# Kernel optimization log

Measured on AMD Instinct MI355X. Metric: run time of the kernel, lower is better.

Reference implementation:

```python
import jax, jax.numpy as jnp
import numpy as np

NEG = -1e30


def setup_inputs() -> dict:
    key = jax.random.key(0)
    k1, k2, k3, k4 = jax.random.split(key, 4)
    B, L, T, M = 64, 256, 1600, 80
    probs = jax.random.uniform(k1, (B, L, T), dtype=jnp.float32)
    melspec = jax.random.normal(k2, (B, M, T), dtype=jnp.float32)
    text_lengths = jax.random.randint(k3, (B,), 1, L + 1)   # values in [1, L]
    mel_lengths = jax.random.randint(k4, (B,), 1, T + 1)    # values in [1, T]
    return {"probs": probs, "melspec": melspec,
            "text_lengths": text_lengths, "mel_lengths": mel_lengths}


def reference(probs, melspec, text_lengths, mel_lengths):
    B, L, _ = probs.shape
    T = melspec.shape[2]
    log_prob_matrix = jnp.log(probs + 1e-30)            # [B, L, T]
    lp_t = jnp.moveaxis(log_prob_matrix, 2, 0)          # [T, B, L]

    # t = 0: only (l=0, t=0) is alive
    init = jnp.full((B, L), NEG, dtype=log_prob_matrix.dtype)
    init = init.at[:, 0].set(lp_t[0, :, 0])

    def step(prev, lp):
        # stay at label l, or advance from label l-1 (monotonic alignment)
        shifted = jnp.concatenate(
            [jnp.full((B, 1), NEG, dtype=prev.dtype), prev[:, :-1]], axis=1)
        new = jnp.logaddexp(prev, shifted) + lp
        return new, new

    _, ys = jax.lax.scan(step, init, lp_t[1:])          # ys: [T-1, B, L]
    log_alpha = jnp.concatenate([init[None], ys], axis=0)  # [T, B, L]

    b = jnp.arange(B)
    alpha_last = log_alpha[mel_lengths - 1, b, text_lengths - 1]  # [B]
    mdn_loss = -alpha_last.mean()
    return (mdn_loss, log_prob_matrix)
```

## Files before the change

### kernel.cpp

```cpp
#include <hip/hip_runtime.h>

#define LN2f 0.69314718055994531f

constexpr int T_C  = 1600;
constexpr int L_C  = 256;
constexpr int DP_B = 64;
constexpr int CK   = 16;
constexpr int LOGB = 1216;

typedef float f4u __attribute__((ext_vector_type(4), aligned(4)));
typedef float f4a __attribute__((ext_vector_type(4)));

__device__ __forceinline__ float shift_up1_f(float x, bool f15, bool f31) {
    int xi  = __float_as_int(x);
    int s   = __builtin_amdgcn_update_dpp(0, xi, 0x111, 0xF, 0xF, true);
    int b15 = __builtin_amdgcn_update_dpp(0, xi, 0x142, 0xF, 0xF, true);
    int b31 = __builtin_amdgcn_update_dpp(0, xi, 0x143, 0xF, 0xF, true);
    int r = f15 ? b15 : s;
    r     = f31 ? b31 : r;
    return __int_as_float(r);
}
__device__ __forceinline__ int shift_up1_i(int x, bool f15, bool f31) {
    int s   = __builtin_amdgcn_update_dpp(0, x, 0x111, 0xF, 0xF, true);
    int b15 = __builtin_amdgcn_update_dpp(0, x, 0x142, 0xF, 0xF, true);
    int b31 = __builtin_amdgcn_update_dpp(0, x, 0x143, 0xF, 0xF, true);
    int r = f15 ? b15 : s;
    r     = f31 ? b31 : r;
    return r;
}

__global__ __launch_bounds__(256, 5) void fused_kernel(
    const float* __restrict__ probs,
    const int* __restrict__ text_len,
    const int* __restrict__ mel_len,
    float* __restrict__ out1,
    float* __restrict__ alpha_out,
    int n4)
{
    __shared__ float lds[2][CK][L_C];
    const int b   = blockIdx.x;
    const int tid = threadIdx.x;

    if (b >= DP_B) {
        const int W = LOGB * 256;
        const int M = n4 - 1;
        int m = (b - DP_B) * 256 + tid;
        if (m >= M) return;
        const float* src = probs + 3;
        float*       dst = out1 + 3;
        f4u v0 = *(const f4u*)(src + 4 * (size_t)m);
        int  m1 = m + W;
        bool h1 = m1 < M;
        f4u v1 = v0;
        if (h1) v1 = *(const f4u*)(src + 4 * (size_t)m1);
        for (;;) {
            const int  m2 = m1 + W;
            const bool h2 = m2 < M;
            f4u v2;
            if (h2) v2 = *(const f4u*)(src + 4 * (size_t)m2);
            f4a o;
            o.x = __logf(v0.x + 1e-30f);
            o.y = __logf(v0.y + 1e-30f);
            o.z = __logf(v0.z + 1e-30f);
            o.w = __logf(v0.w + 1e-30f);
            __builtin_nontemporal_store(o, (f4a*)(dst + 4 * (size_t)m));
            if (!h1) return;
            v0 = v1; v1 = v2; m = m1; m1 = m2; h1 = h2;
        }
    }

    const int wv   = tid >> 6;
    const int lane = tid & 63;
    const int ml1  = mel_len[b] - 1;
    const int trip = (ml1 >> 4) + 1;

    if (wv != 0) {
        asm volatile("s_setprio 1");
        const int pw   = wv - 1;
        const int q    = lane & 3;
        const int g    = lane >> 2;
        const int row0 = pw * 16 + g;
        const int NIT  = (pw == 0) ? 6 : 5;
        const float* gbase = probs + (size_t)b * (L_C * T_C)
                           + (size_t)row0 * T_C + q * 4;
        const int swz = 8 * q;

        float4 rA[6], rB[6];
        auto LD = [&](float4 (&r)[6], int ck) {
            const float* p = gbase + ck * CK;
#pragma unroll
            for (int it = 0; it < 6; ++it)
                if (it < NIT) r[it] = *(const float4*)(p + it * (48 * T_C));
        };
        auto WR = [&](float4 (&r)[6], int bb) {
            float* Lw = &lds[bb][0][0];
#pragma unroll
            for (int it = 0; it < 6; ++it) {
                if (it < NIT) {
                    const int A0 = q * 1024 + ((row0 + 48 * it) ^ swz);
                    Lw[A0]             = r[it].x + 1e-30f;
                    Lw[A0 + 256]       = r[it].y + 1e-30f;
                    Lw[(A0 ^ 4) + 512] = r[it].z + 1e-30f;
                    Lw[(A0 ^ 4) + 768] = r[it].w + 1e-30f;
                }
            }
        };

        LD(rA, 0);
        if (trip > 1) LD(rB, 1);
        WR(rA, 0);
        for (int w = 0; w < trip; ++w) {
            __syncthreads();
            if ((w & 1) == 0) {
                if (w + 2 < trip) LD(rA, w + 2);
                if (w + 1 < trip) WR(rB, 1);
            } else {
                if (w + 2 < trip) LD(rB, w + 2);
                if (w + 1 < trip) WR(rA, 0);
            }
        }
        return;
    }

    asm volatile("s_setprio 3");
    const int  cl  = text_len[b] - 1;
    const bool f15 = (lane == 16) | (lane == 48);
    const bool f31 = (lane == 32);
    const int  xr  = 4 * lane;

    float a0 = 0.f, a1 = 0.f, a2 = 0.f, a3 = 0.f;
    int   E = 0;
    bool  alive = (lane == 0);
    float s0 = 0.f, s1 = 0.f, s2 = 0.f, s3 = 0.f;
    int   sE = 0;

    auto renorm = [&]() {
        float m = fmaxf(fmaxf(a0, a1), fmaxf(a2, a3));
        int e = ((__float_as_int(m) >> 23) & 255) - 127;
        e = (m > 0.0f) ? e : 0;
        a0 = ldexpf(a0, -e); a1 = ldexpf(a1, -e);
        a2 = ldexpf(a2, -e); a3 = ldexpf(a3, -e);
        E += e;
    };

    for (int w = 0; w < trip; ++w) {
        __syncthreads();
        const float* Lr = &lds[w & 1][0][0];
        const int tb = w << 4;

        auto ldc = [&](int j) -> float4 {
            return *(const float4*)(Lr + j * 256 + (xr ^ (4 * ((j >> 1) & 7))));
        };
        auto step_full = [&](int j) {
            const float4 c = ldc(j);
            float top = shift_up1_f(a3, f15, f31);
            int   tE  = shift_up1_i(E, f15, f31);
            float contrib = alive ? ldexpf(top, tE - E) : top;
            E = alive ? E : tE;
            alive = alive | (top != 0.0f);
            float n0 = (a0 + contrib) * c.x;
            float n1 = (a1 + a0) * c.y;
            float n2 = (a2 + a1) * c.z;
            float n3 = (a3 + a2) * c.w;
            a0 = n0; a1 = n1; a2 = n2; a3 = n3;
            if (tb + j == ml1) { s0 = a0; s1 = a1; s2 = a2; s3 = a3; sE = E; }
        };

        if (w == 0) {
            const float4 c = ldc(0);
            a0 = (lane == 0) ? c.x : 0.0f;
            if (ml1 == 0) s0 = a0;
#pragma unroll
            for (int j = 1; j < CK; ++j) step_full(j);
            renorm();
        } else if (w < 16) {
#pragma unroll
            for (int j = 0; j < CK; ++j) step_full(j);
            renorm();
        } else {
            const int tE = shift_up1_i(E, f15, f31);
            const int dE = tE - E;
            if (w == trip - 1) {
#pragma unroll
                for (int j = 0; j < CK; ++j) {
                    const float4 c = ldc(j);
                    float top = shift_up1_f(a3, f15, f31);
                    float contrib = ldexpf(top, dE);
                    float n0 = (a0 + contrib) * c.x;
                    float n1 = (a1 + a0) * c.y;
                    float n2 = (a2 + a1) * c.z;
                    float n3 = (a3 + a2) * c.w;
                    a0 = n0; a1 = n1; a2 = n2; a3 = n3;
                    if (tb + j == ml1) { s0 = a0; s1 = a1; s2 = a2; s3 = a3; sE = E; }
                }
            } else {
#pragma unroll
                for (int j = 0; j < CK; ++j) {
                    const float4 c = ldc(j);
                    float top = shift_up1_f(a3, f15, f31);
                    float contrib = ldexpf(top, dE);
                    float n0 = (a0 + contrib) * c.x;
                    float n1 = (a1 + a0) * c.y;
                    float n2 = (a2 + a1) * c.z;
                    float n3 = (a3 + a2) * c.w;
                    a0 = n0; a1 = n1; a2 = n2; a3 = n3;
                }
            }
            renorm();
        }
    }

    if (lane == (cl >> 2)) {
        const int jj = cl & 3;
        float v = (jj == 0) ? s0 : (jj == 1) ? s1 : (jj == 2) ? s2 : s3;
        v = fmaxf(v, 1e-44f);
        const float res = (log2f(v) + (float)sE) * LN2f;
        alpha_out[b] = (cl > ml1) ? -1e30f : res;
    }
}

__global__ void loss_kernel(const float* __restrict__ alpha,
                            const float* __restrict__ probs,
                            float* __restrict__ out, int B, int n) {
    const int t = threadIdx.x;
    if (t < 3)  out[1 + t] = __logf(probs[t] + 1e-30f);
    if (t == 3) out[n] = __logf(probs[n - 1] + 1e-30f);
    float v = (t < B) ? alpha[t] : 0.0f;
#pragma unroll
    for (int off = 32; off > 0; off >>= 1) v += __shfl_down(v, off, 64);
    if (t == 0) out[0] = -v / (float)B;
}

extern "C" void kernel_launch(void* const* d_in, const int* in_sizes, int n_in,
                              void* d_out, int out_size, void* d_ws, size_t ws_size,
                              hipStream_t stream) {
    const float* probs    = (const float*)d_in[0];
    const int*   text_len = (const int*)d_in[2];
    const int*   mel_len  = (const int*)d_in[3];
    float* out = (float*)d_out;

    const int B  = in_sizes[2];
    const int n  = in_sizes[0];
    const int n4 = n / 4;
    const int G  = DP_B + LOGB;

    fused_kernel<<<G, 256, 0, stream>>>(probs, text_len, mel_len,
                                        out + 1, (float*)d_ws, n4);
    loss_kernel<<<1, 64, 0, stream>>>((const float*)d_ws, probs, out, B, n);
}
```

Baseline: 270.2 us.

## Deepen producer prefetch to three register stages and batch LDS reads per chunk

The producer waves now keep three register buffers of global loads in flight, prefetching chunk w+3 instead of w+2, so more global latency is hidden behind the serial DP wave. The consumer wave loads all 16 LDS float4 columns of a chunk into registers up front, behind a scheduling barrier, instead of reading each inside the dependent recurrence step. This takes LDS latency off the serial critical path. In exchange, register pressure rises in both roles, which could cause spills or hurt occupancy under the 256x5 launch bounds.

```diff
diff --git a/kernel.cpp b/kernel.cpp
--- a/kernel.cpp
+++ b/kernel.cpp
@@ -85,7 +85,7 @@
                            + (size_t)row0 * T_C + q * 4;
         const int swz = 8 * q;
 
-        float4 rA[6], rB[6];
+        float4 rA[6], rB[6], rC[6];
         auto LD = [&](float4 (&r)[6], int ck) {
             const float* p = gbase + ck * CK;
 #pragma unroll
@@ -108,16 +108,23 @@
 
         LD(rA, 0);
         if (trip > 1) LD(rB, 1);
+        if (trip > 2) LD(rC, 2);
         WR(rA, 0);
+        int ph = 0;
         for (int w = 0; w < trip; ++w) {
             __syncthreads();
-            if ((w & 1) == 0) {
-                if (w + 2 < trip) LD(rA, w + 2);
-                if (w + 1 < trip) WR(rB, 1);
+            const int bb = (w + 1) & 1;
+            if (ph == 0) {
+                if (w + 3 < trip) LD(rA, w + 3);
+                if (w + 1 < trip) WR(rB, bb);
+            } else if (ph == 1) {
+                if (w + 3 < trip) LD(rB, w + 3);
+                if (w + 1 < trip) WR(rC, bb);
             } else {
-                if (w + 2 < trip) LD(rB, w + 2);
-                if (w + 1 < trip) WR(rA, 0);
+                if (w + 3 < trip) LD(rC, w + 3);
+                if (w + 1 < trip) WR(rA, bb);
             }
+            ph = (ph == 2) ? 0 : ph + 1;
         }
         return;
     }
@@ -148,27 +155,28 @@
         const float* Lr = &lds[w & 1][0][0];
         const int tb = w << 4;
 
-        auto ldc = [&](int j) -> float4 {
-            return *(const float4*)(Lr + j * 256 + (xr ^ (4 * ((j >> 1) & 7))));
-        };
+        float4 c[CK];
+#pragma unroll
+        for (int j = 0; j < CK; ++j)
+            c[j] = *(const float4*)(Lr + j * 256 + (xr ^ (4 * ((j >> 1) & 7))));
+        __builtin_amdgcn_sched_barrier(0);
+
         auto step_full = [&](int j) {
-            const float4 c = ldc(j);
             float top = shift_up1_f(a3, f15, f31);
             int   tE  = shift_up1_i(E, f15, f31);
             float contrib = alive ? ldexpf(top, tE - E) : top;
             E = alive ? E : tE;
             alive = alive | (top != 0.0f);
-            float n0 = (a0 + contrib) * c.x;
-            float n1 = (a1 + a0) * c.y;
-            float n2 = (a2 + a1) * c.z;
-            float n3 = (a3 + a2) * c.w;
+            float n0 = (a0 + contrib) * c[j].x;
+            float n1 = (a1 + a0) * c[j].y;
+            float n2 = (a2 + a1) * c[j].z;
+            float n3 = (a3 + a2) * c[j].w;
             a0 = n0; a1 = n1; a2 = n2; a3 = n3;
             if (tb + j == ml1) { s0 = a0; s1 = a1; s2 = a2; s3 = a3; sE = E; }
         };
 
         if (w == 0) {
-            const float4 c = ldc(0);
-            a0 = (lane == 0) ? c.x : 0.0f;
+            a0 = (lane == 0) ? c[0].x : 0.0f;
             if (ml1 == 0) s0 = a0;
 #pragma unroll
             for (int j = 1; j < CK; ++j) step_full(j);
@@ -183,26 +191,24 @@
             if (w == trip - 1) {
 #pragma unroll
                 for (int j = 0; j < CK; ++j) {
-                    const float4 c = ldc(j);
                     float top = shift_up1_f(a3, f15, f31);
                     float contrib = ldexpf(top, dE);
-                    float n0 = (a0 + contrib) * c.x;
-                    float n1 = (a1 + a0) * c.y;
-                    float n2 = (a2 + a1) * c.z;
-                    float n3 = (a3 + a2) * c.w;
+                    float n0 = (a0 + contrib) * c[j].x;
+                    float n1 = (a1 + a0) * c[j].y;
+                    float n2 = (a2 + a1) * c[j].z;
+                    float n3 = (a3 + a2) * c[j].w;
                     a0 = n0; a1 = n1; a2 = n2; a3 = n3;
                     if (tb + j == ml1) { s0 = a0; s1 = a1; s2 = a2; s3 = a3; sE = E; }
                 }
             } else {
 #pragma unroll
                 for (int j = 0; j < CK; ++j) {
-                    const float4 c = ldc(j);
                     float top = shift_up1_f(a3, f15, f31);
                     float contrib = ldexpf(top, dE);
-                    float n0 = (a0 + contrib) * c.x;
-                    float n1 = (a1 + a0) * c.y;
-                    float n2 = (a2 + a1) * c.z;
-                    float n3 = (a3 + a2) * c.w;
+                    float n0 = (a0 + contrib) * c[j].x;
+                    float n1 = (a1 + a0) * c[j].y;
+                    float n2 = (a2 + a1) * c[j].z;
+                    float n3 = (a3 + a2) * c[j].w;
                     a0 = n0; a1 = n1; a2 = n2; a3 = n3;
                 }
             }
```

Result: slower. 516.4 us (+91.1%).
